# Kernel tuning notes

Measured on AMD Instinct MI355X. Metric: run time of the kernel, lower is better.

Reference implementation:

```python
import jax, jax.numpy as jnp
import numpy as np
import math

B, T, N, C = 1, 12, 10000, 32
TIME_DIM, N_SUP, E, NODE_EMB = 8, 3, 320000, 32
S = N_SUP + 2  # support_len + 2 slots after concat


def setup_inputs() -> dict:
    key = jax.random.key(0)
    ks = jax.random.split(key, 16)
    inp = {
        'x': jax.random.normal(ks[0], (B, T, N, C), jnp.float32),
        'timeoh': jax.random.uniform(ks[1], (B, 43), jnp.float32),
        'edges': jax.random.randint(ks[2], (N_SUP, 2, E), 0, N),
        # shared dy_gat params (attention_list reuses the same ModuleList)
        'mlp_w': jax.random.normal(ks[3], (C, C), jnp.float32) * 0.05,
        'mlp_b': jnp.zeros((C,), jnp.float32),
        'temb_w': jax.random.normal(ks[4], (43, TIME_DIM), jnp.float32) * 0.1,
        'atten_pool': jax.random.normal(ks[5], (TIME_DIM, 2 * C), jnp.float32) * 0.1,
        # adaptive-adjacency gcn branch
        'node2vec': jax.random.normal(ks[6], (N, NODE_EMB), jnp.float32) * 0.1,
        'gcn_w': jax.random.normal(ks[7], (3 * C, C), jnp.float32) * 0.05,
        'gcn_b': jnp.zeros((C,), jnp.float32),
        # slot self-attention over S supports
        'q_w': jax.random.normal(ks[8], (C, 6 * C), jnp.float32) * 0.05,
        'q_b': jnp.zeros((6 * C,), jnp.float32),
        'k_w': jax.random.normal(ks[9], (C, 6 * C), jnp.float32) * 0.05,
        'k_b': jnp.zeros((6 * C,), jnp.float32),
        'v_w': jax.random.normal(ks[10], (C, 6 * C), jnp.float32) * 0.05,
        'v_b': jnp.zeros((6 * C,), jnp.float32),
        'dense_w': jax.random.normal(ks[11], (6 * C, C), jnp.float32) * 0.05,
        'dense_b': jnp.zeros((C,), jnp.float32),
    }
    return inp


def _dy_gat(x, timeoh, src, dst, mlp_w, mlp_b, temb_w, atten_pool):
    h = x @ mlp_w + mlp_b                                   # (B,T,N,C)
    attn = (timeoh @ temb_w) @ atten_pool                    # (B,2C)
    # einsum('btnc,bc->btn') over concatenated [h_src, h_dst] splits additively
    s_src = jnp.einsum('btnc,bc->btn', h, attn[:, :C])
    s_dst = jnp.einsum('btnc,bc->btn', h, attn[:, C:])
    values = s_src[:, :, src] + s_dst[:, :, dst]             # (B,T,E)
    p = jax.nn.leaky_relu(values, 0.01)
    e = jnp.exp(p - jnp.max(p, axis=2, keepdims=True))       # global (per b,t) max-shift
    rowsum = jnp.zeros((B, T, N), e.dtype).at[:, :, src].add(e)
    h_prime = jnp.zeros_like(h).at[:, :, src].add(e[..., None] * h[:, :, dst, :])
    h_prime = h_prime / (rowsum[..., None] + 9e-15)
    return jax.nn.elu(h_prime)  # concat=True


def reference(x, timeoh, edges, mlp_w, mlp_b, temb_w, atten_pool,
              node2vec, gcn_w, gcn_b, q_w, q_b, k_w, k_b, v_w, v_b,
              dense_w, dense_b):
    outs = [x]
    for i in range(N_SUP):
        outs.append(_dy_gat(x, timeoh, edges[i, 0], edges[i, 1],
                            mlp_w, mlp_b, temb_w, atten_pool))
    # adaptive graph conv (static, order=2, support_len=1)
    adj = jax.nn.softmax(jax.nn.relu(node2vec @ node2vec.T), axis=1)  # (N,N)
    x1 = jnp.einsum('wv,btvf->btwf', adj, x)
    x2 = jnp.einsum('wv,btvf->btwf', adj, x1)
    x_adp = jnp.concatenate([x, x1, x2], -1) @ gcn_w + gcn_b
    outs.append(x_adp)
    out = jnp.concatenate(outs, -1).reshape(B, T, N, S, C)
    q = out @ q_w + q_b                                       # (B,T,N,S,6C)
    k = out @ k_w + k_b
    v = out @ v_w + v_b
    scores = jnp.einsum('btnsd,btnud->btnsu', q, k) / math.sqrt(6 * C)
    a = jax.nn.softmax(scores, axis=-1)
    o = jnp.einsum('btnsu,btnud->btnsd', a, v)
    o = o @ dense_w + dense_b                                 # (B,T,N,S,C)
    return jax.nn.elu(jnp.mean(o, axis=-2))                   # (B,T,N,C)
```

## Files before the change

kernel.cpp:

```cpp
#include <hip/hip_runtime.h>
#include <hip/hip_bf16.h>

#define T_ 12
#define N_ 10000
#define C_ 32
#define E_ 320000
#define SUP_ 3
#define TN_ (T_*N_)

typedef __attribute__((ext_vector_type(4))) float f32x4;
typedef __attribute__((ext_vector_type(8))) short bf16x8;
typedef __attribute__((ext_vector_type(4))) short bf16x4;

__device__ __forceinline__ short bf16c(float f) {
  __hip_bfloat16 b = __float2bfloat16(f);
  return (short)__builtin_bit_cast(unsigned short, b);
}

#if __has_builtin(__builtin_amdgcn_exp2f)
#define EXP2F(x) __builtin_amdgcn_exp2f(x)
#else
#define EXP2F(x) exp2f(x)
#endif

#define PRM_ATTN 0
#define PRM_G    64
#define PRM_H    1088
#define PRM_G1   2112
#define PRM_G2   2144
#define PRM_HB   2176
#define PRM_G0   2208

__global__ __launch_bounds__(256) void k_prep(
    const float* __restrict__ timeoh, const float* __restrict__ temb_w,
    const float* __restrict__ atten_pool,
    const float* __restrict__ q_w, const float* __restrict__ q_b,
    const float* __restrict__ k_w, const float* __restrict__ k_b,
    const float* __restrict__ v_w, const float* __restrict__ v_b,
    const float* __restrict__ dense_w, const float* __restrict__ dense_b,
    float* __restrict__ prm) {
  __shared__ float tv[8];
  int tid = threadIdx.x;
  if (tid < 8) {
    float s = 0.f;
    for (int j = 0; j < 43; j++) s += timeoh[j] * temb_w[j * 8 + tid];
    tv[tid] = s;
  }
  __syncthreads();
  if (tid < 64) {
    float s = 0.f;
    for (int d = 0; d < 8; d++) s += tv[d] * atten_pool[d * 64 + tid];
    prm[PRM_ATTN + tid] = s;
  }
  for (int idx = tid; idx < 1024; idx += 256) {
    int r = idx >> 5, c = idx & 31;
    float s = 0.f, s2 = 0.f;
    for (int d = 0; d < 192; d++) {
      s  += q_w[r * 192 + d] * k_w[c * 192 + d];
      s2 += v_w[r * 192 + d] * dense_w[d * 32 + c];
    }
    prm[PRM_G + idx] = s;
    prm[PRM_H + idx] = s2;
  }
  if (tid < 32) {
    float s = 0.f, s2 = 0.f, s3 = 0.f;
    for (int d = 0; d < 192; d++) {
      s  += q_w[tid * 192 + d] * k_b[d];
      s2 += k_w[tid * 192 + d] * q_b[d];
      s3 += v_b[d] * dense_w[d * 32 + tid];
    }
    prm[PRM_G1 + tid] = s;
    prm[PRM_G2 + tid] = s2;
    prm[PRM_HB + tid] = s3 + dense_b[tid];
  }
  if (tid == 0) {
    float s = 0.f;
    for (int d = 0; d < 192; d++) s += q_b[d] * k_b[d];
    prm[PRM_G0] = s;
  }
}

__global__ __launch_bounds__(256) void k_h(
    const float* __restrict__ x, const float* __restrict__ mlp_w,
    const float* __restrict__ mlp_b, const float* __restrict__ prm,
    __hip_bfloat16* __restrict__ h16, float* __restrict__ s_src,
    float* __restrict__ s_dst) {
  __shared__ float W[32 * 32];
  __shared__ float bsh[32], attnsh[64];
  __shared__ float xs[8][32];
  int tid = threadIdx.x;
  for (int i = tid; i < 1024; i += 256) W[i] = mlp_w[i];
  if (tid < 32) bsh[tid] = mlp_b[tid];
  if (tid < 64) attnsh[tid] = prm[PRM_ATTN + tid];
  long base = (long)blockIdx.x * 8;
  int nloc = tid >> 5, c = tid & 31;
  long row = base + nloc;
  xs[nloc][c] = x[row * 32 + c];
  __syncthreads();
  float hval = bsh[c];
#pragma unroll
  for (int k = 0; k < 32; k++) hval = fmaf(xs[nloc][k], W[k * 32 + c], hval);
  h16[row * 32 + c] = __float2bfloat16(hval);
  float a = hval * attnsh[c], b = hval * attnsh[32 + c];
#pragma unroll
  for (int m = 16; m >= 1; m >>= 1) {
    a += __shfl_xor(a, m, 64);
    b += __shfl_xor(b, m, 64);
  }
  if (c == 0) { s_src[row] = a; s_dst[row] = b; }
}

__global__ __launch_bounds__(256) void k_maxs(const float* __restrict__ ssrc,
                                              const float* __restrict__ sdst,
                                              float* __restrict__ Mt) {
  __shared__ float sh[8];
  const int t = blockIdx.x, tid = threadIdx.x;
  float ma = -1e30f, mb = -1e30f;
  for (int i = tid; i < N_; i += 256) {
    ma = fmaxf(ma, ssrc[(long)t * N_ + i]);
    mb = fmaxf(mb, sdst[(long)t * N_ + i]);
  }
#pragma unroll
  for (int k = 32; k >= 1; k >>= 1) {
    ma = fmaxf(ma, __shfl_xor(ma, k, 64));
    mb = fmaxf(mb, __shfl_xor(mb, k, 64));
  }
  if ((tid & 63) == 0) { sh[(tid >> 6) * 2] = ma; sh[(tid >> 6) * 2 + 1] = mb; }
  __syncthreads();
  if (tid == 0) {
    float A = fmaxf(fmaxf(sh[0], sh[2]), fmaxf(sh[4], sh[6]));
    float B = fmaxf(fmaxf(sh[1], sh[3]), fmaxf(sh[5], sh[7]));
    Mt[t] = A + B;
  }
}

__global__ __launch_bounds__(256) void k_hist(const int* __restrict__ edges,
                                              int* __restrict__ cnt) {
  int sup = blockIdx.y;
  int e = blockIdx.x * 256 + threadIdx.x;
  const int* src = edges + (long)sup * 2 * E_;
  atomicAdd(&cnt[sup * N_ + src[e]], 1);
}

__global__ __launch_bounds__(1024) void k_scan(const int* __restrict__ cnt,
                                               int* __restrict__ offs,
                                               int* __restrict__ cur) {
  __shared__ int sh[1024];
  __shared__ int run;
  int sup = blockIdx.x, tid = threadIdx.x;
  if (tid == 0) run = 0;
  __syncthreads();
  for (int base = 0; base < N_; base += 1024) {
    int i = base + tid;
    int v = (i < N_) ? cnt[sup * N_ + i] : 0;
    sh[tid] = v;
    __syncthreads();
    for (int off = 1; off < 1024; off <<= 1) {
      int t = (tid >= off) ? sh[tid - off] : 0;
      __syncthreads();
      sh[tid] += t;
      __syncthreads();
    }
    int runv = run;
    int excl = runv + sh[tid] - v;
    if (i < N_) {
      offs[sup * (N_ + 1) + i] = excl;
      cur[sup * N_ + i] = excl;
    }
    __syncthreads();
    if (tid == 0) run = runv + sh[1023];
    __syncthreads();
  }
  if (tid == 0) offs[sup * (N_ + 1) + N_] = run;
}

__global__ __launch_bounds__(256) void k_fill(const int* __restrict__ edges,
                                              int* __restrict__ cur,
                                              int* __restrict__ csr) {
  int sup = blockIdx.y;
  int e = blockIdx.x * 256 + threadIdx.x;
  const int* src = edges + (long)sup * 2 * E_;
  const int* dst = src + E_;
  int pos = atomicAdd(&cur[sup * N_ + src[e]], 1);
  csr[sup * E_ + pos] = dst[e];
}

__global__ __launch_bounds__(256) void k_gather(
    const int* __restrict__ csr, const int* __restrict__ offs,
    const float* __restrict__ s_src, const float* __restrict__ s_dst,
    const float* __restrict__ Mt, const __hip_bfloat16* __restrict__ h16,
    __hip_bfloat16* __restrict__ hp16) {
  const int sup = blockIdx.z, t = blockIdx.y;
  const int wave = threadIdx.x >> 6, lane = threadIdx.x & 63;
  const int n = blockIdx.x * 4 + wave;
  const float M = Mt[t];
  const float a = s_src[(long)t * N_ + n];
  const int off = offs[sup * (N_ + 1) + n], end = offs[sup * (N_ + 1) + n + 1];
  const float* sd = s_dst + (long)t * N_;
  const uint4* hb4 = (const uint4*)(h16 + (long)t * N_ * 32);
  const int* csrs = csr + sup * E_;
  const int slot = lane >> 2, cl = lane & 3;
  const int clamp = (end > off) ? (end - 1) : 0;

  float acc[8];
#pragma unroll
  for (int j = 0; j < 8; j++) acc[j] = 0.f;
  float psum = 0.f;

  const int idx0 = off + slot;
  int d0 = csrs[min(idx0, clamp)];
  int d1 = csrs[min(idx0 + 16, clamp)];
  float sd0 = sd[d0];
  uint4 u0 = hb4[d0 * 4 + cl];

  for (int idx = idx0; idx < end; idx += 16) {
    int d2 = csrs[min(idx + 32, clamp)];
    float sd1 = sd[d1];
    uint4 u1 = hb4[d1 * 4 + cl];
    float v = a + sd0;
    v = fmaxf(v, 0.01f * v);
    float p = __expf(v - M);
    psum += p;
    acc[0] = fmaf(p, __uint_as_float(u0.x << 16),        acc[0]);
    acc[1] = fmaf(p, __uint_as_float(u0.x & 0xffff0000u), acc[1]);
    acc[2] = fmaf(p, __uint_as_float(u0.y << 16),        acc[2]);
    acc[3] = fmaf(p, __uint_as_float(u0.y & 0xffff0000u), acc[3]);
    acc[4] = fmaf(p, __uint_as_float(u0.z << 16),        acc[4]);
    acc[5] = fmaf(p, __uint_as_float(u0.z & 0xffff0000u), acc[5]);
    acc[6] = fmaf(p, __uint_as_float(u0.w << 16),        acc[6]);
    acc[7] = fmaf(p, __uint_as_float(u0.w & 0xffff0000u), acc[7]);
    d1 = d2; sd0 = sd1; u0 = u1;
  }

#pragma unroll
  for (int m = 4; m <= 32; m <<= 1) psum += __shfl_xor(psum, m, 64);
#pragma unroll
  for (int j = 0; j < 8; j++) {
#pragma unroll
    for (int m = 4; m <= 32; m <<= 1) acc[j] += __shfl_xor(acc[j], m, 64);
  }

  if (slot == 0) {
    float inv = 1.f / (psum + 9e-15f);
    unsigned w[4];
#pragma unroll
    for (int q = 0; q < 4; q++) {
      float h0 = acc[2 * q + 0] * inv;
      float h1 = acc[2 * q + 1] * inv;
      h0 = (h0 > 0.f) ? h0 : (__expf(h0) - 1.f);
      h1 = (h1 > 0.f) ? h1 : (__expf(h1) - 1.f);
      unsigned lo = (unsigned)(unsigned short)__builtin_bit_cast(unsigned short, __float2bfloat16(h0));
      unsigned hi = (unsigned)(unsigned short)__builtin_bit_cast(unsigned short, __float2bfloat16(h1));
      w[q] = lo | (hi << 16);
    }
    ((uint4*)hp16)[((long)sup * TN_ + (long)t * N_ + n) * 4 + cl] = uint4{w[0], w[1], w[2], w[3]};
  }
}

__global__ __launch_bounds__(256) void k_n2vA(const float* __restrict__ n2v,
                                              short* __restrict__ n2vA) {
  const float SC = 1.2011224087864498f;
  int idx = blockIdx.x * 256 + threadIdx.x;
  if (idx >= N_ * 4) return;
  int row = idx >> 2, l4 = idx & 3;
  short v[8];
#pragma unroll
  for (int h = 0; h < 2; h++)
#pragma unroll
    for (int j = 0; j < 4; j++)
      v[h * 4 + j] = bf16c(n2v[row * 32 + 16 * h + 4 * l4 + j] * SC);
  *(bf16x8*)&n2vA[(long)idx * 8] = bf16x8{v[0], v[1], v[2], v[3], v[4], v[5], v[6], v[7]};
}

template <int WITHR>
__global__ __launch_bounds__(256) void k_pack(const float* __restrict__ src,
                                              const float* __restrict__ rinv,
                                              short* __restrict__ xq) {
  int idx = blockIdx.x * 256 + threadIdx.x;
  int ck = idx / 1536;
  int rem = idx - ck * 1536;
  int l4 = rem / 384;
  int col = rem - l4 * 384;
  int t = col >> 5, f = col & 31;
  const long cb = (long)t * N_ * 32 + f;
  short v[8];
#pragma unroll
  for (int e = 0; e < 8; e++) {
    int vv = ck * 32 + 4 * l4 + (e & 3) + 16 * (e >> 2);
    float a = 0.f;
    if (vv < N_) {
      a = src[cb + (long)vv * 32];
      if (WITHR) a *= rinv[vv];
    }
    v[e] = bf16c(a);
  }
  *(bf16x8*)&xq[(long)idx * 8] = bf16x8{v[0], v[1], v[2], v[3], v[4], v[5], v[6], v[7]};
}

template <int PASS>
__global__ __launch_bounds__(512, 2) void k_adj12(const short* __restrict__ n2vA,
                                                  const short* __restrict__ xq,
                                                  float* __restrict__ out,
                                                  float* __restrict__ Rout) {
  __shared__ __align__(16) short aPl[2][8 * 4 * 64 * 8];
  const int tid = threadIdx.x;
  const int lane = tid & 63;
  const int wv = tid >> 6;
  const int l15 = lane & 15;
  const int l4 = lane >> 4;
  const int brow0 = blockIdx.x * 64;
  const int colbase = wv * 48;

  bf16x8 bw[4];
#pragma unroll
  for (int mt = 0; mt < 4; mt++) {
    int row = brow0 + mt * 16 + l15;
    row = row < N_ ? row : N_ - 1;
    bw[mt] = *(const bf16x8*)&n2vA[((long)row * 4 + l4) * 8];
  }

  f32x4 acc[4][3];
#pragma unroll
  for (int i = 0; i < 4; i++)
#pragma unroll
    for (int j = 0; j < 3; j++) acc[i][j] = f32x4{0.f, 0.f, 0.f, 0.f};
  float racc[4] = {0.f, 0.f, 0.f, 0.f};

#define PHASE_A(cexpr, slab)                                                              \
  {                                                                                       \
    const int c_ = (cexpr);                                                               \
    if (c_ < 313) {                                                                       \
      const int vb_ = c_ * 32;                                                            \
      int r1_ = vb_ + 16 + l15; r1_ = r1_ < N_ ? r1_ : N_ - 1;                            \
      bf16x8 av0_ = *(const bf16x8*)&n2vA[((long)(vb_ + l15) * 4 + l4) * 8];              \
      bf16x8 av1_ = *(const bf16x8*)&n2vA[((long)r1_ * 4 + l4) * 8];                      \
      _Pragma("unroll")                                                                   \
      for (int mt = 0; mt < 4; mt++) {                                                    \
        f32x4 s0_ = __builtin_amdgcn_mfma_f32_16x16x32_bf16(av0_, bw[mt],                 \
                                                            f32x4{0.f,0.f,0.f,0.f},0,0,0);\
        f32x4 s1_ = __builtin_amdgcn_mfma_f32_16x16x32_bf16(av1_, bw[mt],                 \
                                                            f32x4{0.f,0.f,0.f,0.f},0,0,0);\
        short pp_[8];                                                                     \
        float rs0_ = 0.f, rs1_ = 0.f;                                                     \
        _Pragma("unroll")                                                                 \
        for (int j = 0; j < 4; j++) {                                                     \
          float p0_ = EXP2F(fmaxf(s0_[j], 0.f));                                          \
          float p1_ = EXP2F(fmaxf(s1_[j], 0.f));                                          \
          if constexpr (PASS == 1) { rs0_ += p0_; rs1_ += p1_; }                          \
          pp_[j] = bf16c(p0_);                                                            \
          pp_[j + 4] = bf16c(p1_);                                                        \
        }                                                                                 \
        *(bf16x8*)&aPl[slab][((wv * 4 + mt) * 64 + lane) * 8] =                           \
            bf16x8{pp_[0],pp_[1],pp_[2],pp_[3],pp_[4],pp_[5],pp_[6],pp_[7]};              \
        if constexpr (PASS == 1) racc[mt] += (c_ != 312) ? (rs0_ + rs1_) : rs0_;          \
      }                                                                                   \
    }                                                                                     \
  }

  PHASE_A(wv, 0)
  __syncthreads();

  for (int g = 0; g < 40; g++) {
    const int cur = g & 1;
    if (g + 1 < 40) PHASE_A((g + 1) * 8 + wv, cur ^ 1)

    const int rem = 313 - g * 8;
    if (rem >= 8) {
      bf16x8 bx[24];
#pragma unroll
      for (int cc = 0; cc < 8; cc++) {
        const long xb = (long)(g * 8 + cc) * 1536 + (long)l4 * 384;
        bx[cc * 3 + 0] = *(const bf16x8*)&xq[(xb + colbase + 0 * 16 + l15) * 8];
        bx[cc * 3 + 1] = *(const bf16x8*)&xq[(xb + colbase + 1 * 16 + l15) * 8];
        bx[cc * 3 + 2] = *(const bf16x8*)&xq[(xb + colbase + 2 * 16 + l15) * 8];
      }
#pragma unroll
      for (int cc = 0; cc < 8; cc++) {
#pragma unroll
        for (int mt = 0; mt < 4; mt++) {
          bf16x8 aP = *(const bf16x8*)&aPl[cur][((cc * 4 + mt) * 64 + lane) * 8];
          acc[mt][0] = __builtin_amdgcn_mfma_f32_16x16x32_bf16(aP, bx[cc * 3 + 0], acc[mt][0], 0, 0, 0);
          acc[mt][1] = __builtin_amdgcn_mfma_f32_16x16x32_bf16(aP, bx[cc * 3 + 1], acc[mt][1], 0, 0, 0);
          acc[mt][2] = __builtin_amdgcn_mfma_f32_16x16x32_bf16(aP, bx[cc * 3 + 2], acc[mt][2], 0, 0, 0);
        }
      }
    } else {
      for (int cc = 0; cc < rem; cc++) {
        const long xb = (long)(g * 8 + cc) * 1536 + (long)l4 * 384;
        bf16x8 bx0 = *(const bf16x8*)&xq[(xb + colbase + 0 * 16 + l15) * 8];
        bf16x8 bx1 = *(const bf16x8*)&xq[(xb + colbase + 1 * 16 + l15) * 8];
        bf16x8 bx2 = *(const bf16x8*)&xq[(xb + colbase + 2 * 16 + l15) * 8];
#pragma unroll
        for (int mt = 0; mt < 4; mt++) {
          bf16x8 aP = *(const bf16x8*)&aPl[cur][((cc * 4 + mt) * 64 + lane) * 8];
          acc[mt][0] = __builtin_amdgcn_mfma_f32_16x16x32_bf16(aP, bx0, acc[mt][0], 0, 0, 0);
          acc[mt][1] = __builtin_amdgcn_mfma_f32_16x16x32_bf16(aP, bx1, acc[mt][1], 0, 0, 0);
          acc[mt][2] = __builtin_amdgcn_mfma_f32_16x16x32_bf16(aP, bx2, acc[mt][2], 0, 0, 0);
        }
      }
    }
    __syncthreads();
  }
#undef PHASE_A

  if constexpr (PASS == 1) {
#pragma unroll
    for (int mt = 0; mt < 4; mt++) {
      float r = racc[mt];
      r += __shfl_xor(r, 16, 64);
      r += __shfl_xor(r, 32, 64);
      int w = brow0 + mt * 16 + l15;
      if (l4 == 0 && w < N_) atomicAdd(&Rout[w], r);
    }
  }
#pragma unroll
  for (int mt = 0; mt < 4; mt++) {
#pragma unroll
    for (int nt = 0; nt < 3; nt++) {
      const int col = colbase + nt * 16 + l15;
      const int t = col >> 5, f = col & 31;
#pragma unroll
      for (int j = 0; j < 4; j++) {
        const int w = brow0 + mt * 16 + 4 * l4 + j;
        if (w < N_) out[((long)t * N_ + w) * 32 + f] = acc[mt][nt][j];
      }
    }
  }
}

__global__ __launch_bounds__(256) void k_rinv(float* __restrict__ R) {
  int i = blockIdx.x * 256 + threadIdx.x;
  if (i < N_) R[i] = 1.f / R[i];
}

__global__ __launch_bounds__(256) void k_gcn(const float* __restrict__ x,
                                             const float* __restrict__ x1,
                                             float* __restrict__ x2io,
                                             const float* __restrict__ Rinv,
                                             const float* __restrict__ gcn_w,
                                             const float* __restrict__ gcn_b) {
  __shared__ float W[96 * 32];
  __shared__ float bsh[32];
  __shared__ float rows[8][96];
  int tid = threadIdx.x;
  for (int i = tid; i < 96 * 32; i += 256) W[i] = gcn_w[i];
  if (tid < 32) bsh[tid] = gcn_b[tid];
  long base = (long)blockIdx.x * 8;
  int nloc = tid >> 5, c = tid & 31;
  long row = base + nloc;
  long nIdx = row % N_;
  float ri = Rinv[nIdx];
  rows[nloc][c] = x[row * 32 + c];
  rows[nloc][32 + c] = x1[row * 32 + c] * ri;
  rows[nloc][64 + c] = x2io[row * 32 + c] * ri;
  __syncthreads();
  float o = bsh[c];
#pragma unroll
  for (int k = 0; k < 96; k++) o = fmaf(rows[nloc][k], W[k * 32 + c], o);
  __syncthreads();
  x2io[row * 32 + c] = o;
}

__device__ __forceinline__ void load_row(int s, long r, const float* __restrict__ x,
                                         const __hip_bfloat16* __restrict__ hp16,
                                         const float* __restrict__ xadp, float* m) {
  if (s == 0 || s == 4) {
    const float4* p = (const float4*)((s == 0 ? x : xadp) + r * 32);
#pragma unroll
    for (int q = 0; q < 8; q++) {
      float4 v = p[q];
      m[q * 4 + 0] = v.x; m[q * 4 + 1] = v.y; m[q * 4 + 2] = v.z; m[q * 4 + 3] = v.w;
    }
  } else {
    const uint4* p = (const uint4*)(hp16 + ((long)(s - 1) * TN_ + r) * 32);
#pragma unroll
    for (int q = 0; q < 4; q++) {
      uint4 v = p[q];
      unsigned uu[4] = {v.x, v.y, v.z, v.w};
#pragma unroll
      for (int j = 0; j < 4; j++) {
        m[q * 8 + j * 2 + 0] = __uint_as_float(uu[j] << 16);
        m[q * 8 + j * 2 + 1] = __uint_as_float(uu[j] & 0xffff0000u);
      }
    }
  }
}

__global__ __launch_bounds__(256) void k_attn(const float* __restrict__ x,
                                              const __hip_bfloat16* __restrict__ hp16,
                                              const float* __restrict__ xadp,
                                              const float* __restrict__ prm,
                                              float* __restrict__ out) {
  __shared__ float Gs[1024], Hs[1024], g1s[32], g2s[32], hbs[32];
  __shared__ float g0sh;
  int tid = threadIdx.x;
  for (int i = tid; i < 1024; i += 256) { Gs[i] = prm[PRM_G + i]; Hs[i] = prm[PRM_H + i]; }
  if (tid < 32) { g1s[tid] = prm[PRM_G1 + tid]; g2s[tid] = prm[PRM_G2 + tid]; hbs[tid] = prm[PRM_HB + tid]; }
  if (tid == 0) g0sh = prm[PRM_G0];
  __syncthreads();
  long r = (long)blockIdx.x * 256 + tid;
  if (r >= TN_) return;
  float g0 = g0sh;
  float sc[5][5], d1[5], d2[5];
  float ms[32], mu[32], y[32];
#pragma unroll
  for (int s = 0; s < 5; s++) {
    load_row(s, r, x, hp16, xadp, ms);
    float a = 0.f, b = 0.f;
#pragma unroll
    for (int k = 0; k < 32; k++) { a = fmaf(ms[k], g1s[k], a); b = fmaf(ms[k], g2s[k], b); }
    d1[s] = a; d2[s] = b;
#pragma unroll
    for (int c = 0; c < 32; c++) {
      float s2 = 0.f;
#pragma unroll
      for (int k = 0; k < 32; k++) s2 = fmaf(ms[k], Gs[k * 32 + c], s2);
      y[c] = s2;
    }
#pragma unroll
    for (int u = 0; u < 5; u++) {
      load_row(u, r, x, hp16, xadp, mu);
      float dt = 0.f;
#pragma unroll
      for (int k = 0; k < 32; k++) dt = fmaf(y[k], mu[k], dt);
      sc[s][u] = dt;
    }
  }
  const float rs = 0.07216878364870322f;
  float abar[5];
#pragma unroll
  for (int u = 0; u < 5; u++) abar[u] = 0.f;
#pragma unroll
  for (int s = 0; s < 5; s++) {
    float e[5];
    float mx = -1e30f;
#pragma unroll
    for (int u = 0; u < 5; u++) {
      float v = (sc[s][u] + d1[s] + d2[u] + g0) * rs;
      e[u] = v;
      mx = fmaxf(mx, v);
    }
    float sm = 0.f;
#pragma unroll
    for (int u = 0; u < 5; u++) { e[u] = __expf(e[u] - mx); sm += e[u]; }
    float inv = 1.f / sm;
#pragma unroll
    for (int u = 0; u < 5; u++) abar[u] = fmaf(e[u], inv, abar[u]);
  }
  float z[32];
#pragma unroll
  for (int k = 0; k < 32; k++) z[k] = 0.f;
#pragma unroll
  for (int u = 0; u < 5; u++) {
    load_row(u, r, x, hp16, xadp, mu);
    float w = abar[u] * 0.2f;
#pragma unroll
    for (int k = 0; k < 32; k++) z[k] = fmaf(w, mu[k], z[k]);
  }
#pragma unroll
  for (int c = 0; c < 32; c++) {
    float o = hbs[c];
#pragma unroll
    for (int k = 0; k < 32; k++) o = fmaf(z[k], Hs[k * 32 + c], o);
    o = (o > 0.f) ? o : (__expf(o) - 1.f);
    out[r * 32 + c] = o;
  }
}

extern "C" void kernel_launch(void* const* d_in, const int* in_sizes, int n_in,
                              void* d_out, int out_size, void* d_ws, size_t ws_size,
                              hipStream_t stream) {
  (void)in_sizes; (void)n_in; (void)out_size; (void)ws_size;
  const float* x          = (const float*)d_in[0];
  const float* timeoh     = (const float*)d_in[1];
  const int*   edges      = (const int*)d_in[2];
  const float* mlp_w      = (const float*)d_in[3];
  const float* mlp_b      = (const float*)d_in[4];
  const float* temb_w     = (const float*)d_in[5];
  const float* atten_pool = (const float*)d_in[6];
  const float* node2vec   = (const float*)d_in[7];
  const float* gcn_w      = (const float*)d_in[8];
  const float* gcn_b      = (const float*)d_in[9];
  const float* q_w  = (const float*)d_in[10];
  const float* q_b  = (const float*)d_in[11];
  const float* k_w  = (const float*)d_in[12];
  const float* k_b  = (const float*)d_in[13];
  const float* v_w  = (const float*)d_in[14];
  const float* v_b  = (const float*)d_in[15];
  const float* dense_w = (const float*)d_in[16];
  const float* dense_b = (const float*)d_in[17];
  float* out = (float*)d_out;
  char* ws = (char*)d_ws;

  float*    prm  = (float*)(ws + 0);
  float*    Mt   = (float*)(ws + 9216);
  int*      cnt  = (int*)(ws + 9472);
  int*      cur  = (int*)(ws + 129472);
  int*      offs = (int*)(ws + 249472);
  float*    ssrc = (float*)(ws + 369664);
  float*    sdst = (float*)(ws + 849664);
  float*    R    = (float*)(ws + 1329664);
  __hip_bfloat16* h16  = (__hip_bfloat16*)(ws + 1369664);
  int*      csr  = (int*)(ws + 9049664);
  __hip_bfloat16* hp16 = (__hip_bfloat16*)(ws + 12889664);
  float*    x1   = (float*)(ws + 35929664);
  float*    x2   = (float*)(ws + 51289664);
  short*    n2vA = (short*)(ws + 66649664);
  short*    xq0  = (short*)(ws + 67289664);
  short*    xq1  = (short*)(ws + 74983488);

  (void)hipMemsetAsync(cnt, 0, 120000, stream);
  (void)hipMemsetAsync(R, 0, 40000, stream);

  k_prep<<<1, 256, 0, stream>>>(timeoh, temb_w, atten_pool, q_w, q_b, k_w, k_b,
                                v_w, v_b, dense_w, dense_b, prm);
  k_h<<<15000, 256, 0, stream>>>(x, mlp_w, mlp_b, prm, h16, ssrc, sdst);
  k_maxs<<<12, 256, 0, stream>>>(ssrc, sdst, Mt);
  k_hist<<<dim3(1250, 3), 256, 0, stream>>>(edges, cnt);
  k_scan<<<3, 1024, 0, stream>>>(cnt, offs, cur);
  k_fill<<<dim3(1250, 3), 256, 0, stream>>>(edges, cur, csr);
  k_gather<<<dim3(2500, 12, 3), 256, 0, stream>>>(csr, offs, ssrc, sdst, Mt, h16, hp16);

  k_n2vA<<<157, 256, 0, stream>>>(node2vec, n2vA);
  k_pack<0><<<1878, 256, 0, stream>>>(x, nullptr, xq0);
  k_adj12<1><<<157, 512, 0, stream>>>(n2vA, xq0, x1, R);
  k_rinv<<<40, 256, 0, stream>>>(R);
  k_pack<1><<<1878, 256, 0, stream>>>(x1, R, xq1);
  k_adj12<2><<<157, 512, 0, stream>>>(n2vA, xq1, x2, nullptr);
  k_gcn<<<15000, 256, 0, stream>>>(x, x1, x2, R, gcn_w, gcn_b);
  k_attn<<<469, 256, 0, stream>>>(x, hp16, x2, prm, out);
}
```

Measured before the change: 843.5 us.

## Parallelize slot attention across lanes per row with shuffle reductions

Replaces the one-thread-per-row attention kernel with a version where 32 lanes cooperate on each row, staging the five slot rows in shared memory. Dot products become lane-parallel with xor-shuffle reductions, and the final dense projection reads the averaged vector from shared memory. This removes the large per-thread register arrays and repeated row reloads that limited occupancy, at the cost of many shuffles and more blocks.

```diff
diff --git a/kernel.cpp b/kernel.cpp
--- a/kernel.cpp
+++ b/kernel.cpp
@@ -461,72 +461,61 @@
   x2io[row * 32 + c] = o;
 }
 
-__device__ __forceinline__ void load_row(int s, long r, const float* __restrict__ x,
-                                         const __hip_bfloat16* __restrict__ hp16,
-                                         const float* __restrict__ xadp, float* m) {
-  if (s == 0 || s == 4) {
-    const float4* p = (const float4*)((s == 0 ? x : xadp) + r * 32);
-#pragma unroll
-    for (int q = 0; q < 8; q++) {
-      float4 v = p[q];
-      m[q * 4 + 0] = v.x; m[q * 4 + 1] = v.y; m[q * 4 + 2] = v.z; m[q * 4 + 3] = v.w;
-    }
-  } else {
-    const uint4* p = (const uint4*)(hp16 + ((long)(s - 1) * TN_ + r) * 32);
-#pragma unroll
-    for (int q = 0; q < 4; q++) {
-      uint4 v = p[q];
-      unsigned uu[4] = {v.x, v.y, v.z, v.w};
-#pragma unroll
-      for (int j = 0; j < 4; j++) {
-        m[q * 8 + j * 2 + 0] = __uint_as_float(uu[j] << 16);
-        m[q * 8 + j * 2 + 1] = __uint_as_float(uu[j] & 0xffff0000u);
-      }
-    }
-  }
-}
-
-__global__ __launch_bounds__(256) void k_attn(const float* __restrict__ x,
-                                              const __hip_bfloat16* __restrict__ hp16,
-                                              const float* __restrict__ xadp,
-                                              const float* __restrict__ prm,
-                                              float* __restrict__ out) {
+__global__ __launch_bounds__(256) void k_attn2(const float* __restrict__ x,
+                                               const __hip_bfloat16* __restrict__ hp16,
+                                               const float* __restrict__ xadp,
+                                               const float* __restrict__ prm,
+                                               float* __restrict__ out) {
   __shared__ float Gs[1024], Hs[1024], g1s[32], g2s[32], hbs[32];
   __shared__ float g0sh;
-  int tid = threadIdx.x;
+  __shared__ float msl[8][5][33];
+  __shared__ float zl[8][33];
+  const int tid = threadIdx.x;
+  const int nloc = tid >> 5, c = tid & 31;
   for (int i = tid; i < 1024; i += 256) { Gs[i] = prm[PRM_G + i]; Hs[i] = prm[PRM_H + i]; }
   if (tid < 32) { g1s[tid] = prm[PRM_G1 + tid]; g2s[tid] = prm[PRM_G2 + tid]; hbs[tid] = prm[PRM_HB + tid]; }
   if (tid == 0) g0sh = prm[PRM_G0];
-  __syncthreads();
-  long r = (long)blockIdx.x * 256 + tid;
-  if (r >= TN_) return;
-  float g0 = g0sh;
-  float sc[5][5], d1[5], d2[5];
-  float ms[32], mu[32], y[32];
+  const long r = (long)blockIdx.x * 8 + nloc;
+  msl[nloc][0][c] = x[r * 32 + c];
+#pragma unroll
+  for (int s = 1; s <= 3; s++)
+    msl[nloc][s][c] = __bfloat162float(hp16[((long)(s - 1) * TN_ + r) * 32 + c]);
+  msl[nloc][4][c] = xadp[r * 32 + c];
+  __syncthreads();
+
+  float msr[5];
+#pragma unroll
+  for (int s = 0; s < 5; s++) msr[s] = msl[nloc][s][c];
+
+  float d1[5], d2[5];
 #pragma unroll
   for (int s = 0; s < 5; s++) {
-    load_row(s, r, x, hp16, xadp, ms);
-    float a = 0.f, b = 0.f;
-#pragma unroll
-    for (int k = 0; k < 32; k++) { a = fmaf(ms[k], g1s[k], a); b = fmaf(ms[k], g2s[k], b); }
+    float a = msr[s] * g1s[c], b = msr[s] * g2s[c];
+#pragma unroll
+    for (int m = 1; m <= 16; m <<= 1) {
+      a += __shfl_xor(a, m, 64);
+      b += __shfl_xor(b, m, 64);
+    }
     d1[s] = a; d2[s] = b;
-#pragma unroll
-    for (int c = 0; c < 32; c++) {
-      float s2 = 0.f;
-#pragma unroll
-      for (int k = 0; k < 32; k++) s2 = fmaf(ms[k], Gs[k * 32 + c], s2);
-      y[c] = s2;
-    }
+  }
+
+  float sc[5][5];
+#pragma unroll
+  for (int s = 0; s < 5; s++) {
+    float y = 0.f;
+#pragma unroll
+    for (int k = 0; k < 32; k++) y = fmaf(msl[nloc][s][k], Gs[k * 32 + c], y);
 #pragma unroll
     for (int u = 0; u < 5; u++) {
-      load_row(u, r, x, hp16, xadp, mu);
-      float dt = 0.f;
-#pragma unroll
-      for (int k = 0; k < 32; k++) dt = fmaf(y[k], mu[k], dt);
+      float dt = y * msr[u];
+#pragma unroll
+      for (int m = 1; m <= 16; m <<= 1) dt += __shfl_xor(dt, m, 64);
       sc[s][u] = dt;
     }
   }
+
   const float rs = 0.07216878364870322f;
+  const float g0 = g0sh;
   float abar[5];
 #pragma unroll
   for (int u = 0; u < 5; u++) abar[u] = 0.f;
@@ -547,24 +536,17 @@
 #pragma unroll
     for (int u = 0; u < 5; u++) abar[u] = fmaf(e[u], inv, abar[u]);
   }
-  float z[32];
-#pragma unroll
-  for (int k = 0; k < 32; k++) z[k] = 0.f;
-#pragma unroll
-  for (int u = 0; u < 5; u++) {
-    load_row(u, r, x, hp16, xadp, mu);
-    float w = abar[u] * 0.2f;
-#pragma unroll
-    for (int k = 0; k < 32; k++) z[k] = fmaf(w, mu[k], z[k]);
-  }
-#pragma unroll
-  for (int c = 0; c < 32; c++) {
-    float o = hbs[c];
-#pragma unroll
-    for (int k = 0; k < 32; k++) o = fmaf(z[k], Hs[k * 32 + c], o);
-    o = (o > 0.f) ? o : (__expf(o) - 1.f);
-    out[r * 32 + c] = o;
-  }
+
+  float z = 0.f;
+#pragma unroll
+  for (int u = 0; u < 5; u++) z = fmaf(abar[u], msr[u], z);
+  zl[nloc][c] = z * 0.2f;
+
+  float o = hbs[c];
+#pragma unroll
+  for (int k = 0; k < 32; k++) o = fmaf(zl[nloc][k], Hs[k * 32 + c], o);
+  o = (o > 0.f) ? o : (__expf(o) - 1.f);
+  out[r * 32 + c] = o;
 }
 
 extern "C" void kernel_launch(void* const* d_in, const int* in_sizes, int n_in,
@@ -613,7 +595,7 @@
   (void)hipMemsetAsync(R, 0, 40000, stream);
 
   k_prep<<<1, 256, 0, stream>>>(timeoh, temb_w, atten_pool, q_w, q_b, k_w, k_b,
-                                v_w, v_b, dense_w, dense_b, prm);
+                                v_b ? v_w : v_w, v_b, dense_w, dense_b, prm);
   k_h<<<15000, 256, 0, stream>>>(x, mlp_w, mlp_b, prm, h16, ssrc, sdst);
   k_maxs<<<12, 256, 0, stream>>>(ssrc, sdst, Mt);
   k_hist<<<dim3(1250, 3), 256, 0, stream>>>(edges, cnt);
@@ -628,5 +610,5 @@
   k_pack<1><<<1878, 256, 0, stream>>>(x1, R, xq1);
   k_adj12<2><<<157, 512, 0, stream>>>(n2vA, xq1, x2, nullptr);
   k_gcn<<<15000, 256, 0, stream>>>(x, x1, x2, R, gcn_w, gcn_b);
-  k_attn<<<469, 256, 0, stream>>>(x, hp16, x2, prm, out);
-}
+  k_attn2<<<15000, 256, 0, stream>>>(x, hp16, x2, prm, out);
+}
```

Result: slower. 938.8 us (+11.3%).

## Store h and scores node-major so one wave gathers all timesteps per edge

Applied to the files above, without the earlier changes.

k_h now writes h16 and the src/dst scores transposed to node-major [n][t] order. k_gather drops the time grid dimension: each wave handles one node across all 12 timesteps (48 lanes), walking edges serially, so each neighbour's 12×32 bf16 row is read as one contiguous 768-byte chunk and the CSR index is loaded once instead of 12 times. The cross-lane shuffle reduction is removed. In exchange, each node's edge loop runs serially with one edge per iteration instead of 16 in parallel, so there is less memory-level parallelism per wave. 16 of the 64 lanes sit idle, and k_maxs now reads with a stride of 12.

```diff
diff --git a/kernel.cpp b/kernel.cpp
--- a/kernel.cpp
+++ b/kernel.cpp
@@ -83,8 +83,8 @@
 __global__ __launch_bounds__(256) void k_h(
     const float* __restrict__ x, const float* __restrict__ mlp_w,
     const float* __restrict__ mlp_b, const float* __restrict__ prm,
-    __hip_bfloat16* __restrict__ h16, float* __restrict__ s_src,
-    float* __restrict__ s_dst) {
+    __hip_bfloat16* __restrict__ h16t, float* __restrict__ s_srct,
+    float* __restrict__ s_dstt) {
   __shared__ float W[32 * 32];
   __shared__ float bsh[32], attnsh[64];
   __shared__ float xs[8][32];
@@ -95,30 +95,32 @@
   long base = (long)blockIdx.x * 8;
   int nloc = tid >> 5, c = tid & 31;
   long row = base + nloc;
+  const int t = (int)(row / N_);
+  const int n = (int)(row - (long)t * N_);
   xs[nloc][c] = x[row * 32 + c];
   __syncthreads();
   float hval = bsh[c];
 #pragma unroll
   for (int k = 0; k < 32; k++) hval = fmaf(xs[nloc][k], W[k * 32 + c], hval);
-  h16[row * 32 + c] = __float2bfloat16(hval);
+  h16t[((long)n * 12 + t) * 32 + c] = __float2bfloat16(hval);
   float a = hval * attnsh[c], b = hval * attnsh[32 + c];
 #pragma unroll
   for (int m = 16; m >= 1; m >>= 1) {
     a += __shfl_xor(a, m, 64);
     b += __shfl_xor(b, m, 64);
   }
-  if (c == 0) { s_src[row] = a; s_dst[row] = b; }
-}
-
-__global__ __launch_bounds__(256) void k_maxs(const float* __restrict__ ssrc,
-                                              const float* __restrict__ sdst,
+  if (c == 0) { s_srct[(long)n * 12 + t] = a; s_dstt[(long)n * 12 + t] = b; }
+}
+
+__global__ __launch_bounds__(256) void k_maxs(const float* __restrict__ ssrct,
+                                              const float* __restrict__ sdstt,
                                               float* __restrict__ Mt) {
   __shared__ float sh[8];
   const int t = blockIdx.x, tid = threadIdx.x;
   float ma = -1e30f, mb = -1e30f;
   for (int i = tid; i < N_; i += 256) {
-    ma = fmaxf(ma, ssrc[(long)t * N_ + i]);
-    mb = fmaxf(mb, sdst[(long)t * N_ + i]);
+    ma = fmaxf(ma, ssrct[(long)i * 12 + t]);
+    mb = fmaxf(mb, sdstt[(long)i * 12 + t]);
   }
 #pragma unroll
   for (int k = 32; k >= 1; k >>= 1) {
@@ -187,19 +189,19 @@
 
 __global__ __launch_bounds__(256) void k_gather(
     const int* __restrict__ csr, const int* __restrict__ offs,
-    const float* __restrict__ s_src, const float* __restrict__ s_dst,
-    const float* __restrict__ Mt, const __hip_bfloat16* __restrict__ h16,
+    const float* __restrict__ s_srct, const float* __restrict__ s_dstt,
+    const float* __restrict__ Mt, const __hip_bfloat16* __restrict__ h16t,
     __hip_bfloat16* __restrict__ hp16) {
-  const int sup = blockIdx.z, t = blockIdx.y;
+  const int sup = blockIdx.y;
   const int wave = threadIdx.x >> 6, lane = threadIdx.x & 63;
   const int n = blockIdx.x * 4 + wave;
-  const float M = Mt[t];
-  const float a = s_src[(long)t * N_ + n];
+  const int tg = (lane < 48) ? (lane >> 2) : 0;
+  const int cl = lane & 3;
+  const float at = s_srct[(long)n * 12 + tg];
+  const float Mv = Mt[tg];
   const int off = offs[sup * (N_ + 1) + n], end = offs[sup * (N_ + 1) + n + 1];
-  const float* sd = s_dst + (long)t * N_;
-  const uint4* hb4 = (const uint4*)(h16 + (long)t * N_ * 32);
+  const uint4* hb4 = (const uint4*)h16t;
   const int* csrs = csr + sup * E_;
-  const int slot = lane >> 2, cl = lane & 3;
   const int clamp = (end > off) ? (end - 1) : 0;
 
   float acc[8];
@@ -207,40 +209,31 @@
   for (int j = 0; j < 8; j++) acc[j] = 0.f;
   float psum = 0.f;
 
-  const int idx0 = off + slot;
-  int d0 = csrs[min(idx0, clamp)];
-  int d1 = csrs[min(idx0 + 16, clamp)];
-  float sd0 = sd[d0];
-  uint4 u0 = hb4[d0 * 4 + cl];
-
-  for (int idx = idx0; idx < end; idx += 16) {
-    int d2 = csrs[min(idx + 32, clamp)];
-    float sd1 = sd[d1];
-    uint4 u1 = hb4[d1 * 4 + cl];
-    float v = a + sd0;
+  int d0 = csrs[min(off, clamp)];
+  int d1 = csrs[min(off + 1, clamp)];
+  float sd0 = s_dstt[(long)d0 * 12 + tg];
+  uint4 u0 = hb4[((long)d0 * 12 + tg) * 4 + cl];
+
+  for (int idx = off; idx < end; idx++) {
+    int d2 = csrs[min(idx + 2, clamp)];
+    float sd1 = s_dstt[(long)d1 * 12 + tg];
+    uint4 u1 = hb4[((long)d1 * 12 + tg) * 4 + cl];
+    float v = at + sd0;
     v = fmaxf(v, 0.01f * v);
-    float p = __expf(v - M);
+    float p = __expf(v - Mv);
     psum += p;
-    acc[0] = fmaf(p, __uint_as_float(u0.x << 16),        acc[0]);
+    acc[0] = fmaf(p, __uint_as_float(u0.x << 16),         acc[0]);
     acc[1] = fmaf(p, __uint_as_float(u0.x & 0xffff0000u), acc[1]);
-    acc[2] = fmaf(p, __uint_as_float(u0.y << 16),        acc[2]);
+    acc[2] = fmaf(p, __uint_as_float(u0.y << 16),         acc[2]);
     acc[3] = fmaf(p, __uint_as_float(u0.y & 0xffff0000u), acc[3]);
-    acc[4] = fmaf(p, __uint_as_float(u0.z << 16),        acc[4]);
+    acc[4] = fmaf(p, __uint_as_float(u0.z << 16),         acc[4]);
     acc[5] = fmaf(p, __uint_as_float(u0.z & 0xffff0000u), acc[5]);
-    acc[6] = fmaf(p, __uint_as_float(u0.w << 16),        acc[6]);
+    acc[6] = fmaf(p, __uint_as_float(u0.w << 16),         acc[6]);
     acc[7] = fmaf(p, __uint_as_float(u0.w & 0xffff0000u), acc[7]);
     d1 = d2; sd0 = sd1; u0 = u1;
   }
 
-#pragma unroll
-  for (int m = 4; m <= 32; m <<= 1) psum += __shfl_xor(psum, m, 64);
-#pragma unroll
-  for (int j = 0; j < 8; j++) {
-#pragma unroll
-    for (int m = 4; m <= 32; m <<= 1) acc[j] += __shfl_xor(acc[j], m, 64);
-  }
-
-  if (slot == 0) {
+  if (lane < 48) {
     float inv = 1.f / (psum + 9e-15f);
     unsigned w[4];
 #pragma unroll
@@ -253,7 +246,7 @@
       unsigned hi = (unsigned)(unsigned short)__builtin_bit_cast(unsigned short, __float2bfloat16(h1));
       w[q] = lo | (hi << 16);
     }
-    ((uint4*)hp16)[((long)sup * TN_ + (long)t * N_ + n) * 4 + cl] = uint4{w[0], w[1], w[2], w[3]};
+    ((uint4*)hp16)[((long)sup * TN_ + (long)tg * N_ + n) * 4 + cl] = uint4{w[0], w[1], w[2], w[3]};
   }
 }
 
@@ -619,7 +612,7 @@
   k_hist<<<dim3(1250, 3), 256, 0, stream>>>(edges, cnt);
   k_scan<<<3, 1024, 0, stream>>>(cnt, offs, cur);
   k_fill<<<dim3(1250, 3), 256, 0, stream>>>(edges, cur, csr);
-  k_gather<<<dim3(2500, 12, 3), 256, 0, stream>>>(csr, offs, ssrc, sdst, Mt, h16, hp16);
+  k_gather<<<dim3(2500, 3), 256, 0, stream>>>(csr, offs, ssrc, sdst, Mt, h16, hp16);
 
   k_n2vA<<<157, 256, 0, stream>>>(node2vec, n2vA);
   k_pack<0><<<1878, 256, 0, stream>>>(x, nullptr, xq0);
```

Measured after the change: 804.8 us. -4.6%, faster.
